# Kernel optimization log

Hardware: AMD Instinct MI355X
Metric: run time of the kernel (lower is better)

## Reference

```python
import jax, jax.numpy as jnp
from jax import lax
import numpy as np

# ---- constants matching init_kwargs ----
STEPSZ = 0.1
ALPHA = 0.01
BETA = 0.01
FLTRSTDEV = 2.0
NSTEPS = 20
DMAX = 15.0
EXTGRADFAC = 10.0
THRESH = 0.5
B, H, W = 4, 384, 384
NNODES = 64
ANGLE_STEP = 10  # degrees, as in the source


def make_gauss_edge_fltr(std):
    """Derivative-of-Gaussian edge filters, one per spatial dim -> [2,1,k,k]."""
    r = int(4 * std)
    x = jnp.arange(-r, r + 1, dtype=jnp.float32)
    g = jnp.exp(-0.5 * (x / std) ** 2)
    g = g / g.sum()
    dg = -(x / std ** 2) * jnp.exp(-0.5 * (x / std) ** 2)
    f0 = dg[:, None] * g[None, :]   # d/d(row)
    f1 = g[:, None] * dg[None, :]   # d/d(col)
    return jnp.stack([f0, f1])[:, None]  # [2,1,k,k]


def make_Ainv(n, alpha, beta, stepsz):
    """Implicit-Euler snake internal-energy matrix inverse (I + t*A)^-1 (static)."""
    D1 = np.zeros((n - 1, n), dtype=np.float64)
    for i in range(n - 1):
        D1[i, i], D1[i, i + 1] = -1.0, 1.0
    D2 = np.zeros((n - 2, n), dtype=np.float64)
    for i in range(n - 2):
        D2[i, i], D2[i, i + 1], D2[i, i + 2] = 1.0, -2.0, 1.0
    A = alpha * (D1.T @ D1) + beta * (D2.T @ D2)
    return jnp.asarray(np.linalg.inv(np.eye(n) + stepsz * A), dtype=np.float32)


def bilinear(img, pts):
    """img [C,H,W], pts [N,2] (row,col) -> [N,C] bilinear samples."""
    C, Hh, Ww = img.shape
    x = jnp.clip(pts[:, 0], 0.0, Hh - 1.0)
    y = jnp.clip(pts[:, 1], 0.0, Ww - 1.0)
    x0 = jnp.clip(jnp.floor(x).astype(jnp.int32), 0, Hh - 2)
    y0 = jnp.clip(jnp.floor(y).astype(jnp.int32), 0, Ww - 2)
    fx = (x - x0)[None, :]
    fy = (y - y0)[None, :]
    v00 = img[:, x0, y0]
    v01 = img[:, x0, y0 + 1]
    v10 = img[:, x0 + 1, y0]
    v11 = img[:, x0 + 1, y0 + 1]
    top = v00 * (1 - fy) + v01 * fy
    bot = v10 * (1 - fy) + v11 * fy
    return (top * (1 - fx) + bot * fx).T


def radial_widths(prob, nodes):
    """Vectorized version of the nested r/angle scan: for each node, smallest
    radius r whose ring has an in-bounds pixel with prob < 0.5 -> width r-1;
    if the ring first goes out of bounds with no hit -> width 0."""
    angles = jnp.radians(jnp.arange(0, 360, ANGLE_STEP, dtype=jnp.float32))  # [A]
    rs = jnp.arange(1, H, dtype=jnp.float32)                                 # [R]
    sx = jnp.round(nodes[:, 0])[:, None, None]
    sy = jnp.round(nodes[:, 1])[:, None, None]
    ox = rs[:, None] * jnp.cos(angles)[None, :]  # [R,A]
    oy = rs[:, None] * jnp.sin(angles)[None, :]
    xi = jnp.floor(sx + ox[None]).astype(jnp.int32)  # [N,R,A]
    yi = jnp.floor(sy + oy[None]).astype(jnp.int32)
    inb = (xi >= 0) & (xi < H) & (yi >= 0) & (yi < W)
    p = prob[jnp.clip(xi, 0, H - 1), jnp.clip(yi, 0, W - 1)]
    hit = jnp.any(inb & (p < THRESH), axis=-1)   # [N,R]
    oob = jnp.any(~inb, axis=-1)                 # [N,R]
    stop = hit | oob
    idx = jnp.argmax(stop, axis=-1)              # first stopping radius index
    trig = jnp.any(stop, axis=-1)
    hit_at = jnp.take_along_axis(hit, idx[:, None], axis=-1)[:, 0]
    return jnp.where(trig & hit_at, rs[idx] - 1.0, 0.0)  # [N]


def render_maps(nodes, widths, dmax):
    """Per-pixel min distance to polyline edges (clipped at dmax) and a
    ribbon mask where distance <= linearly-interpolated width."""
    p0, p1 = nodes[:-1], nodes[1:]          # [E,2]
    w0, w1 = widths[:-1], widths[1:]        # [E]
    gx, gy = jnp.meshgrid(jnp.arange(H, dtype=jnp.float32),
                          jnp.arange(W, dtype=jnp.float32), indexing='ij')
    pts = jnp.stack([gx.ravel(), gy.ravel()], axis=-1)  # [P,2]
    v = p1 - p0
    vv = jnp.sum(v * v, axis=-1) + 1e-8
    d = pts[:, None, :] - p0[None, :, :]                # [P,E,2]
    t = jnp.clip(jnp.sum(d * v[None], axis=-1) / vv[None], 0.0, 1.0)  # [P,E]
    proj = p0[None] + t[..., None] * v[None]
    dist = jnp.sqrt(jnp.sum((pts[:, None, :] - proj) ** 2, axis=-1) + 1e-12)
    wt = w0[None] + t * (w1 - w0)[None]
    dmap = jnp.minimum(jnp.min(dist, axis=-1), dmax).reshape(H, W)
    pmap = (jnp.min(dist - wt, axis=-1) <= 0.0).astype(jnp.float32).reshape(H, W)
    return dmap, pmap


def setup_inputs() -> dict:
    key = jax.random.key(0)
    k1, k2 = jax.random.split(key)
    pred_dmap = jax.random.normal(k1, (B, 1, H, W), dtype=jnp.float32)
    # smooth polyline snakes: diagonal-ish curve + jitter, kept in-bounds
    t = jnp.linspace(0.1, 0.9, NNODES)
    base_x = t * (H - 1)
    base_y = (0.5 + 0.2 * jnp.sin(2 * jnp.pi * t)) * (W - 1)
    jitter = (jax.random.uniform(k2, (B, NNODES, 2)) - 0.5) * 8.0
    snake_init = jnp.stack([jnp.broadcast_to(base_x, (B, NNODES)),
                            jnp.broadcast_to(base_y, (B, NNODES))], axis=-1) + jitter
    snake_init = jnp.clip(snake_init, 2.0, H - 3.0).astype(jnp.float32)
    return {"pred_dmap": pred_dmap, "snake_init": snake_init}


def reference(pred_dmap, snake_init):
    fltr = make_gauss_edge_fltr(FLTRSTDEV)
    # gradient image of the predicted distance map, scaled by extgradfac
    gimg = lax.conv_general_dilated(
        pred_dmap, fltr, (1, 1), 'SAME',
        dimension_numbers=('NCHW', 'OIHW', 'NCHW')) * EXTGRADFAC  # [B,2,H,W]
    Ainv = make_Ainv(NNODES, ALPHA, BETA, STEPSZ)

    def per_sample(g, pred_i, nodes0):
        def step(pos, _):
            f = bilinear(g, pos)                     # external force [N,2]
            return Ainv @ (pos + STEPSZ * f), None
        pos, _ = lax.scan(step, nodes0, None, length=NSTEPS)
        prob = jax.nn.sigmoid(-pred_i[0])            # [H,W]
        w = radial_widths(prob, pos)
        return render_maps(pos, w, DMAX)

    dmaps, pmaps = jax.vmap(per_sample)(gimg, pred_dmap, snake_init)
    snake_dm = dmaps[:, None]   # [B,1,H,W]
    ribbon_pm = pmaps[:, None]
    loss = jnp.mean((pred_dmap - snake_dm) ** 2)
    loss = loss + jnp.mean((jax.nn.sigmoid(pred_dmap) - ribbon_pm) ** 2)
    return loss
```

## Files before the change

kernel.cpp:

```cpp
#include <hip/hip_runtime.h>

#define Hh 384
#define Ww 384
#define Bb 4
#define NN 64
#define HW (Hh*Ww)
#define NSEG (NN-1)
#define TPB 24
#define NTILES (TPB*TPB)

struct AinvT { float a[NN][NN]; };
constexpr AinvT make_ainv() {
    AinvT R{};
    float d[NN] = {}, u1[NN] = {}, u2[NN] = {}, b1[NN] = {}, L1[NN] = {}, L2[NN] = {};
    for (int k = 0; k < NN-1; ++k) { d[k] += 0.01f; d[k+1] += 0.01f; u1[k] -= 0.01f; }
    for (int k = 0; k < NN-2; ++k) {
        d[k] += 0.01f; d[k+1] += 0.04f; d[k+2] += 0.01f;
        u1[k] -= 0.02f; u1[k+1] -= 0.02f; u2[k] += 0.01f;
    }
    for (int k = 0; k < NN; ++k) {
        d[k]  = 1.0f + 0.1f*d[k];
        u1[k] = 0.1f*u1[k];
        u2[k] = 0.1f*u2[k];
        b1[k] = u1[k];
    }
    for (int k = 0; k < NN; ++k) {
        float di = d[k];
        if (k+1 < NN) { float l = b1[k]/di; L1[k] = l; d[k+1] -= l*u1[k]; if (k+2 < NN) u1[k+1] -= l*u2[k]; }
        if (k+2 < NN) { float l = u2[k]/di; L2[k] = l; b1[k+1] -= l*u1[k]; d[k+2] -= l*u2[k]; }
    }
    for (int t = 0; t < NN; ++t) {
        float y[NN] = {}, x[NN] = {};
        for (int k = 0; k < NN; ++k) {
            float v = (k == t) ? 1.0f : 0.0f;
            if (k >= 1) v -= L1[k-1]*y[k-1];
            if (k >= 2) v -= L2[k-2]*y[k-2];
            y[k] = v;
        }
        for (int kk = 0; kk < NN; ++kk) {
            int k = NN-1-kk;
            float v = y[k];
            if (k+1 < NN) v -= u1[k]*x[k+1];
            if (k+2 < NN) v -= u2[k]*x[k+2];
            x[k] = v/d[k];
        }
        for (int k = 0; k < NN; ++k) R.a[k][t] = x[k];
    }
    return R;
}
__device__ constexpr AinvT g_Ainv = make_ainv();

#define TILE 32
#define HALO 8
__global__ __launch_bounds__(256) void k_conv(const float* __restrict__ img,
        float2* __restrict__ gimg) {
    __shared__ float sIn[TILE+2*HALO][TILE+2*HALO];
    __shared__ float sColG[TILE+2*HALO][TILE];
    __shared__ float sColD[TILE+2*HALO][TILE];
    __shared__ float gtap[17], dtap[17];
    const int b  = blockIdx.z;
    const int x0 = blockIdx.x * TILE;
    const int y0 = blockIdx.y * TILE;
    const int tid = threadIdx.x;
    if (tid == 0) {
        float s = 0.f;
        for (int i = 0; i < 17; ++i) {
            float xv = (float)(i - 8);
            float e  = expf(-0.5f * (xv*0.5f)*(xv*0.5f));
            gtap[i] = e; s += e;
            dtap[i] = -(xv*0.25f) * e;
        }
        for (int i = 0; i < 17; ++i) gtap[i] /= s;
    }
    const float* im = img + b*HW;
    for (int idx = tid; idx < 48*48; idx += blockDim.x) {
        int r = idx / 48, c = idx % 48;
        int gx = x0 + r - HALO, gy = y0 + c - HALO;
        float v = 0.f;
        if (gx >= 0 && gx < Hh && gy >= 0 && gy < Ww) v = im[gx*Ww + gy];
        sIn[r][c] = v;
    }
    __syncthreads();
    for (int idx = tid; idx < 48*TILE; idx += blockDim.x) {
        int r = idx / TILE, c = idx % TILE;
        float ag = 0.f, ad = 0.f;
#pragma unroll
        for (int k = 0; k < 17; ++k) {
            float v = sIn[r][c+k];
            ag += gtap[k]*v;
            ad += dtap[k]*v;
        }
        sColG[r][c] = ag; sColD[r][c] = ad;
    }
    __syncthreads();
    float2* gg = gimg + (size_t)b*HW;
    for (int idx = tid; idx < TILE*TILE; idx += blockDim.x) {
        int xo = idx / TILE, c = idx % TILE;
        float a0 = 0.f, a1 = 0.f;
#pragma unroll
        for (int k = 0; k < 17; ++k) {
            a0 += dtap[k]*sColG[xo+k][c];
            a1 += gtap[k]*sColD[xo+k][c];
        }
        int gx = x0+xo, gy = y0+c;
        gg[gx*Ww+gy] = make_float2(10.f*a0, 10.f*a1);
    }
}

__global__ __launch_bounds__(256) void k_snake(const float2* __restrict__ gimg,
                        const float* __restrict__ pred, const float* __restrict__ init,
                        float4* __restrict__ pA, float4* __restrict__ pB) {
    __shared__ float2 stxy[NN];
    __shared__ float swf[NN];
    const int b = blockIdx.x;
    const int tid = threadIdx.x;
    const int i = tid >> 2;
    const int q = tid & 3;

    float ar[16];
#pragma unroll
    for (int k = 0; k < 16; ++k) ar[k] = g_Ainv.a[i][q*16 + k];

    float px = init[(b*NN + i)*2 + 0];
    float py = init[(b*NN + i)*2 + 1];
    const float2* g = gimg + (size_t)b*HW;

    for (int s = 0; s < 20; ++s) {
        float x = fminf(fmaxf(px, 0.f), (float)(Hh-1));
        float y = fminf(fmaxf(py, 0.f), (float)(Ww-1));
        int x0i = (int)floorf(x); x0i = min(max(x0i, 0), Hh-2);
        int y0i = (int)floorf(y); y0i = min(max(y0i, 0), Ww-2);
        float fx = x - (float)x0i, fy = y - (float)y0i;
        int base = x0i*Ww + y0i;
        float2 v00 = g[base],    v01 = g[base+1];
        float2 v10 = g[base+Ww], v11 = g[base+Ww+1];
        float t0x = v00.x*(1.f-fy) + v01.x*fy;
        float t0y = v00.y*(1.f-fy) + v01.y*fy;
        float b0x = v10.x*(1.f-fy) + v11.x*fy;
        float b0y = v10.y*(1.f-fy) + v11.y*fy;
        float f0 = t0x*(1.f-fx) + b0x*fx;
        float f1 = t0y*(1.f-fx) + b0y*fx;
        if (q == 0) stxy[i] = make_float2(px + 0.1f*f0, py + 0.1f*f1);
        __syncthreads();
        float ax = 0.f, ay = 0.f;
#pragma unroll
        for (int k = 0; k < 16; ++k) {
            float2 tv = stxy[q*16 + k];
            ax = fmaf(ar[k], tv.x, ax);
            ay = fmaf(ar[k], tv.y, ay);
        }
        ax += __shfl_xor(ax, 1); ay += __shfl_xor(ay, 1);
        ax += __shfl_xor(ax, 2); ay += __shfl_xor(ay, 2);
        px = ax; py = ay;
        __syncthreads();
    }
    if (q == 0) stxy[i] = make_float2(px, py);
    __syncthreads();

    const float* p = pred + (size_t)b*HW;
    const int wid  = tid >> 6;
    const int lane = tid & 63;
    const bool active = lane < 36;
    const float theta = (float)(10*lane) * 0.017453292519943295f;
    const float cth = cosf(theta), sth = sinf(theta);
    for (int nc = 0; nc < 16; ++nc) {
        const int node = wid*16 + nc;
        const float sx = rintf(stxy[node].x);
        const float sy = rintf(stxy[node].y);
        float w = 0.f;
        for (int r = 1; r < Hh; ++r) {
            float rf = (float)r;
            bool hit = false, oob = false;
            if (active) {
                int xi = (int)floorf(sx + rf*cth);
                int yi = (int)floorf(sy + rf*sth);
                bool inb = (xi >= 0) & (xi < Hh) & (yi >= 0) & (yi < Ww);
                if (!inb) oob = true;
                else if (p[xi*Ww + yi] > 0.f) hit = true;
            }
            unsigned long long mh = __ballot(hit);
            unsigned long long mo = __ballot(oob);
            if (mh | mo) { w = mh ? (rf - 1.f) : 0.f; break; }
        }
        if (lane == 0) swf[node] = w;
    }
    __syncthreads();

    if (tid < NSEG) {
        float2 P0 = stxy[tid], P1 = stxy[tid+1];
        float vx = P1.x - P0.x, vy = P1.y - P0.y;
        float vv = vx*vx + vy*vy + 1e-8f;
        float w0 = swf[tid], w1 = swf[tid+1];
        pA[b*NSEG + tid] = make_float4(P0.x, P0.y, vx, vy);
        pB[b*NSEG + tid] = make_float4(1.0f/vv, w0, w1 - w0, 0.f);
    }
}

__global__ __launch_bounds__(256) void k_render(const float* __restrict__ pred,
                        const float4* __restrict__ pAg, const float4* __restrict__ pBg,
                        float* __restrict__ partial) {
    __shared__ float4 sSa[NSEG], sSb[NSEG];
    __shared__ int slist[NSEG];
    __shared__ int scount;
    __shared__ float red[256];
    const int b   = blockIdx.z;
    const int tid = threadIdx.x;
    const int row0 = blockIdx.x * 16, col0 = blockIdx.y * 16;
    if (tid == 0) scount = 0;
    if (tid < NSEG) {
        sSa[tid] = pAg[b*NSEG + tid];
        sSb[tid] = pBg[b*NSEG + tid];
    }
    __syncthreads();
    if (tid < NSEG) {
        const float4 A = sSa[tid];
        const float4 Bv = sSb[tid];
        float cx = (float)row0 + 7.5f, cy = (float)col0 + 7.5f;
        float dx = cx - A.x, dy = cy - A.y;
        float t = fmaf(dy, A.w, dx*A.z) * Bv.x;
        t = fminf(fmaxf(t, 0.f), 1.f);
        float ex = fmaf(-t, A.z, dx);
        float ey = fmaf(-t, A.w, dy);
        float dc = sqrtf(ex*ex + ey*ey);
        float wmax = fmaxf(Bv.y, Bv.y + Bv.z);
        float lim = fmaxf(15.0f, wmax) + 10.6066f + 0.05f;
        if (dc <= lim) {
            int idx = atomicAdd(&scount, 1);
            slist[idx] = tid;
        }
    }
    __syncthreads();
    const int cnt = scount;
    const int r = tid >> 4, c = tid & 15;
    const float fx = (float)(row0 + r), fy = (float)(col0 + c);
    float m1 = 1e30f, m2 = 1e30f;
    for (int k = 0; k < cnt; ++k) {
        const int s2 = slist[k];
        const float4 A = sSa[s2];
        const float4 Bv = sSb[s2];
        float dx = fx - A.x, dy = fy - A.y;
        float t = fmaf(dy, A.w, dx*A.z) * Bv.x;
        t = fminf(fmaxf(t, 0.f), 1.f);
        float ex = fmaf(-t, A.z, dx);
        float ey = fmaf(-t, A.w, dy);
        float d2 = fmaf(ex, ex, fmaf(ey, ey, 1e-12f));
        float wt = fmaf(t, Bv.z, Bv.y);
        m1 = fminf(m1, d2);
        m2 = fminf(m2, fmaf(-wt, wt, d2));
    }
    float dmap = fminf(sqrtf(m1), 15.f);
    float pm = (m2 <= 0.f) ? 1.f : 0.f;
    float pv = pred[(size_t)b*HW + (row0 + r)*Ww + (col0 + c)];
    float sg = 1.f/(1.f + expf(-pv));
    float t1 = pv - dmap, t2 = sg - pm;
    red[tid] = t1*t1 + t2*t2;
    __syncthreads();
    for (int off = 128; off > 0; off >>= 1) {
        if (tid < off) red[tid] += red[tid+off];
        __syncthreads();
    }
    if (tid == 0)
        partial[b*NTILES + blockIdx.y*TPB + blockIdx.x] = red[0];
}

__global__ void k_final(const float* __restrict__ partial, float* __restrict__ out, int n) {
    __shared__ double red[256];
    const int tid = threadIdx.x;
    double a = 0.0;
    for (int i = tid; i < n; i += 256) a += (double)partial[i];
    red[tid] = a; __syncthreads();
    for (int off = 128; off > 0; off >>= 1) {
        if (tid < off) red[tid] += red[tid+off];
        __syncthreads();
    }
    if (tid == 0) out[0] = (float)(red[0] / (double)((size_t)Bb*HW));
}

extern "C" void kernel_launch(void* const* d_in, const int* in_sizes, int n_in,
                              void* d_out, int out_size, void* d_ws, size_t ws_size,
                              hipStream_t stream) {
    const float* pred = (const float*)d_in[0];
    const float* init = (const float*)d_in[1];
    float* out = (float*)d_out;
    char* ws = (char*)d_ws;
    float4* pA     = (float4*)(ws);
    float4* pB     = (float4*)(ws + 4096);
    float* partial = (float*)(ws + 19456);
    float2* gimg   = (float2*)(ws + 28672);

    k_conv  <<<dim3(12,12,4),     dim3(256), 0, stream>>>(pred, gimg);
    k_snake <<<dim3(4),           dim3(256), 0, stream>>>(gimg, pred, init, pA, pB);
    k_render<<<dim3(TPB,TPB,Bb),  dim3(256), 0, stream>>>(pred, pA, pB, partial);
    k_final <<<dim3(1),           dim3(256), 0, stream>>>(partial, out, Bb*NTILES);
}
```

Before: 42.06 us.

## Prefetch first radial ring samples for next node while scanning current node

The radial-width search now speculatively loads the first 8 radii of samples for the next node into registers while the current node's ring hits are evaluated, falling back to the serial per-radius loop only if no hit or out-of-bounds occurs within 8 steps. This is meant to hide the global-load latency of the serial ballot loop behind other work. The snake-step bilinear gather is also restricted to the one lane per node that writes it, cutting redundant loads. The trade-off is more registers and wasted loads when the search ends early.

```diff
diff --git a/kernel.cpp b/kernel.cpp
--- a/kernel.cpp
+++ b/kernel.cpp
@@ -132,15 +132,17 @@
         int y0i = (int)floorf(y); y0i = min(max(y0i, 0), Ww-2);
         float fx = x - (float)x0i, fy = y - (float)y0i;
         int base = x0i*Ww + y0i;
-        float2 v00 = g[base],    v01 = g[base+1];
-        float2 v10 = g[base+Ww], v11 = g[base+Ww+1];
-        float t0x = v00.x*(1.f-fy) + v01.x*fy;
-        float t0y = v00.y*(1.f-fy) + v01.y*fy;
-        float b0x = v10.x*(1.f-fy) + v11.x*fy;
-        float b0y = v10.y*(1.f-fy) + v11.y*fy;
-        float f0 = t0x*(1.f-fx) + b0x*fx;
-        float f1 = t0y*(1.f-fx) + b0y*fx;
-        if (q == 0) stxy[i] = make_float2(px + 0.1f*f0, py + 0.1f*f1);
+        if (q == 0) {
+            float2 v00 = g[base],    v01 = g[base+1];
+            float2 v10 = g[base+Ww], v11 = g[base+Ww+1];
+            float t0x = v00.x*(1.f-fy) + v01.x*fy;
+            float t0y = v00.y*(1.f-fy) + v01.y*fy;
+            float b0x = v10.x*(1.f-fy) + v11.x*fy;
+            float b0y = v10.y*(1.f-fy) + v11.y*fy;
+            float f0 = t0x*(1.f-fx) + b0x*fx;
+            float f1 = t0y*(1.f-fx) + b0y*fx;
+            stxy[i] = make_float2(px + 0.1f*f0, py + 0.1f*f1);
+        }
         __syncthreads();
         float ax = 0.f, ay = 0.f;
 #pragma unroll
@@ -163,27 +165,72 @@
     const bool active = lane < 36;
     const float theta = (float)(10*lane) * 0.017453292519943295f;
     const float cth = cosf(theta), sth = sinf(theta);
+
+    float valA[8], valB[8];
+    unsigned inbA = 0u, inbB = 0u;
+
+#define ISSUE(NC, VAL, INB) { \
+    const int node_ = wid*16 + (NC); \
+    const float sx_ = rintf(stxy[node_].x); \
+    const float sy_ = rintf(stxy[node_].y); \
+    unsigned m_ = 0u; \
+    _Pragma("unroll") \
+    for (int j = 0; j < 8; ++j) { \
+        float rf_ = (float)(j+1); \
+        int xi_ = (int)floorf(sx_ + rf_*cth); \
+        int yi_ = (int)floorf(sy_ + rf_*sth); \
+        bool inb_ = (xi_ >= 0) & (xi_ < Hh) & (yi_ >= 0) & (yi_ < Ww); \
+        m_ |= (inb_ ? 1u : 0u) << j; \
+        int cx_ = min(max(xi_, 0), Hh-1); \
+        int cy_ = min(max(yi_, 0), Ww-1); \
+        VAL[j] = p[cx_*Ww + cy_]; \
+    } \
+    INB = active ? m_ : 0u; }
+
+#define PROCESS(NC, VAL, INB) { \
+    const int node_ = wid*16 + (NC); \
+    float w_ = 0.f; bool done_ = false; \
+    _Pragma("unroll") \
+    for (int j = 0; j < 8; ++j) { \
+        if (!done_) { \
+            bool inb_ = ((INB) >> j) & 1u; \
+            bool hit_ = inb_ && (VAL[j] > 0.f); \
+            bool oob_ = active && !inb_; \
+            unsigned long long mh_ = __ballot(hit_); \
+            unsigned long long mo_ = __ballot(oob_); \
+            if (mh_ | mo_) { w_ = mh_ ? (float)j : 0.f; done_ = true; } \
+        } \
+    } \
+    if (!done_) { \
+        const float sx_ = rintf(stxy[node_].x); \
+        const float sy_ = rintf(stxy[node_].y); \
+        for (int r = 9; r < Hh; ++r) { \
+            float rf_ = (float)r; \
+            bool hit_ = false, oob_ = false; \
+            if (active) { \
+                int xi_ = (int)floorf(sx_ + rf_*cth); \
+                int yi_ = (int)floorf(sy_ + rf_*sth); \
+                bool inb_ = (xi_ >= 0) & (xi_ < Hh) & (yi_ >= 0) & (yi_ < Ww); \
+                if (!inb_) oob_ = true; \
+                else if (p[xi_*Ww + yi_] > 0.f) hit_ = true; \
+            } \
+            unsigned long long mh_ = __ballot(hit_); \
+            unsigned long long mo_ = __ballot(oob_); \
+            if (mh_ | mo_) { w_ = mh_ ? (rf_ - 1.f) : 0.f; break; } \
+        } \
+    } \
+    if (lane == 0) swf[node_] = w_; }
+
+    ISSUE(0, valA, inbA);
     for (int nc = 0; nc < 16; ++nc) {
-        const int node = wid*16 + nc;
-        const float sx = rintf(stxy[node].x);
-        const float sy = rintf(stxy[node].y);
-        float w = 0.f;
-        for (int r = 1; r < Hh; ++r) {
-            float rf = (float)r;
-            bool hit = false, oob = false;
-            if (active) {
-                int xi = (int)floorf(sx + rf*cth);
-                int yi = (int)floorf(sy + rf*sth);
-                bool inb = (xi >= 0) & (xi < Hh) & (yi >= 0) & (yi < Ww);
-                if (!inb) oob = true;
-                else if (p[xi*Ww + yi] > 0.f) hit = true;
-            }
-            unsigned long long mh = __ballot(hit);
-            unsigned long long mo = __ballot(oob);
-            if (mh | mo) { w = mh ? (rf - 1.f) : 0.f; break; }
-        }
-        if (lane == 0) swf[node] = w;
-    }
+        if (nc < 15) ISSUE(nc+1, valB, inbB);
+        PROCESS(nc, valA, inbA);
+#pragma unroll
+        for (int j = 0; j < 8; ++j) valA[j] = valB[j];
+        inbA = inbB;
+    }
+#undef ISSUE
+#undef PROCESS
     __syncthreads();
 
     if (tid < NSEG) {
```

Result: slower. 45.05 us (+7.1%).
